# Kernel optimization log

Hardware: AMD Instinct MI355X
Metric: run time of the kernel (lower is better)

Reference implementation:

```python
import jax, jax.numpy as jnp
import numpy as np

NUM_HEADS = 8
NUM_GROUPS = 8
EPS = 1e-5


def group_norm(x, gamma, beta):
    # x: [B, C, H, W], 8 groups over channel dim
    B, C, H, W = x.shape
    xg = x.reshape(B, NUM_GROUPS, C // NUM_GROUPS, H, W)
    mean = xg.mean(axis=(2, 3, 4), keepdims=True)
    var = xg.var(axis=(2, 3, 4), keepdims=True)
    xn = ((xg - mean) * jax.lax.rsqrt(var + EPS)).reshape(B, C, H, W)
    return xn * gamma[None, :, None, None] + beta[None, :, None, None]


def conv1x1(x, w, b):
    # w: [O, C] (1x1 conv kernel squeezed), x: [B, C, H, W]
    return jnp.einsum('oc,bchw->bohw', w, x) + b[None, :, None, None]


def setup_inputs() -> dict:
    key = jax.random.key(0)
    ks = jax.random.split(key, 6)
    B, C, H, W = 16, 512, 32, 32
    x = jax.random.normal(ks[0], (B, C, H, W), dtype=jnp.float32)
    norm_w = jnp.ones((C,), jnp.float32)
    norm_b = jnp.zeros((C,), jnp.float32)
    s = 1.0 / np.sqrt(C)
    qkv_w = jax.random.uniform(ks[1], (3 * C, C), jnp.float32, -s, s)
    qkv_b = jax.random.uniform(ks[2], (3 * C,), jnp.float32, -s, s)
    proj_w = jax.random.uniform(ks[3], (C, C), jnp.float32, -s, s)
    proj_b = jax.random.uniform(ks[4], (C,), jnp.float32, -s, s)
    return {"x": x, "norm_w": norm_w, "norm_b": norm_b,
            "qkv_w": qkv_w, "qkv_b": qkv_b, "proj_w": proj_w, "proj_b": proj_b}


def reference(x, norm_w, norm_b, qkv_w, qkv_b, proj_w, proj_b):
    B, C, H, W = x.shape
    hd = C // NUM_HEADS  # head dim
    h = group_norm(x, norm_w, norm_b)
    qkv = conv1x1(h, qkv_w, qkv_b)                 # [B, 3C, H, W]
    q, k, v = jnp.split(qkv, 3, axis=1)
    q = q.reshape(B, NUM_HEADS, hd, H * W)
    k = k.reshape(B, NUM_HEADS, hd, H * W)
    v = v.reshape(B, NUM_HEADS, hd, H * W)
    scale = hd ** (-0.5)
    attn = jax.nn.softmax(jnp.einsum('bhci,bhcj->bhij', q, k) * scale, axis=-1)
    h = jnp.einsum('bhij,bhcj->bhci', attn, v).reshape(B, C, H, W)
    h = conv1x1(h, proj_w, proj_b)
    return x + h
```

## Files before the change

### kernel.cpp

```cpp
#include <hip/hip_runtime.h>
#include <hip/hip_bf16.h>


typedef __bf16 bf16;
typedef __attribute__((ext_vector_type(8))) __bf16 bf16x8;
typedef __attribute__((ext_vector_type(4))) float f32x4;
typedef __attribute__((ext_vector_type(16))) float f32x16;
typedef __attribute__((ext_vector_type(4))) unsigned int u32x4;

#define SCALE_Q 0.18033688f

__device__ __forceinline__ bf16x8 ld8(const bf16* p) {
    return *reinterpret_cast<const bf16x8*>(p);
}

__device__ __forceinline__ void gl_lds16(const void* g, void* l) {
    __builtin_amdgcn_global_load_lds(
        (const __attribute__((address_space(1))) void*)g,
        (__attribute__((address_space(3))) void*)l, 16, 0, 0);
}

__global__ __launch_bounds__(256) void cvt_gn(const float* __restrict__ qkv_w,
                                              const float* __restrict__ proj_w,
                                              bf16* __restrict__ wdst,
                                              const float* __restrict__ x,
                                              const float* __restrict__ gamma,
                                              const float* __restrict__ beta,
                                              bf16* __restrict__ hnT) {
    __shared__ float tile[64][65];
    __shared__ float ls[4], lq[4];
    __shared__ float2 st;
    int t = threadIdx.x;
    if (blockIdx.x < 1024) {
        const int N1 = 1536 * 512;
        int i = (blockIdx.x * 256 + t) * 4;
        float4 f = (i < N1) ? *reinterpret_cast<const float4*>(qkv_w + i)
                            : *reinterpret_cast<const float4*>(proj_w + (i - N1));
        wdst[i + 0] = (bf16)f.x;
        wdst[i + 1] = (bf16)f.y;
        wdst[i + 2] = (bf16)f.z;
        wdst[i + 3] = (bf16)f.w;
        return;
    }
    int bg = blockIdx.x - 1024;
    int b = bg >> 3, g = bg & 7;
    const float* base = x + (size_t)bg * 65536;
    int wave = t >> 6, lane = t & 63;

    float s = 0.f, sq = 0.f;
    for (int i = t * 4; i < 65536; i += 256 * 4) {
        float4 f = *reinterpret_cast<const float4*>(base + i);
        s += f.x + f.y + f.z + f.w;
        sq += f.x * f.x + f.y * f.y + f.z * f.z + f.w * f.w;
    }
    #pragma unroll
    for (int off = 32; off > 0; off >>= 1) {
        s += __shfl_down(s, off);
        sq += __shfl_down(sq, off);
    }
    if (lane == 0) { ls[wave] = s; lq[wave] = sq; }
    __syncthreads();
    if (t == 0) {
        s = ls[0] + ls[1] + ls[2] + ls[3];
        sq = lq[0] + lq[1] + lq[2] + lq[3];
        float mean = s * (1.f / 65536.f);
        float var = sq * (1.f / 65536.f) - mean * mean;
        st = make_float2(mean, rsqrtf(var + 1e-5f));
    }
    __syncthreads();
    float mean = st.x, rstd = st.y;

    int cl = t & 63;
    float ga = gamma[g * 64 + cl] * rstd;
    float be = beta[g * 64 + cl] - mean * ga;
    for (int pt = 0; pt < 16; pt++) {
        const float* xb = base + pt * 64;
        #pragma unroll
        for (int r = 0; r < 16; r++) {
            int crow = r * 4 + (t >> 6);
            tile[crow][t & 63] = xb[(size_t)crow * 1024 + (t & 63)];
        }
        __syncthreads();
        bf16* ob = hnT + ((size_t)b * 1024 + pt * 64) * 512 + g * 64 + cl;
        #pragma unroll
        for (int r = 0; r < 16; r++) {
            int pl = r * 4 + (t >> 6);
            ob[(size_t)pl * 512] = (bf16)(tile[cl][pl] * ga + be);
        }
        __syncthreads();
    }
}

__device__ __forceinline__ void gemm_stage(const bf16* __restrict__ A,
                                           const bf16* __restrict__ B,
                                           char* smem, int buf,
                                           int m_blk, int n_blk, int k0,
                                           int wave, int lane) {
    char* Al = smem + buf * 32768;
    char* Bl = Al + 16384;
    #pragma unroll
    for (int i = 0; i < 4; i++) {
        int seg = i * 4 + wave;
        int r = seg * 8 + (lane >> 3);
        int cg = (lane & 7) ^ (r & 7);
        gl_lds16((const char*)(A + (size_t)(m_blk + r) * 512 + k0) + cg * 16,
                 Al + seg * 1024);
        gl_lds16((const char*)(B + (size_t)(n_blk + r) * 512 + k0) + cg * 16,
                 Bl + seg * 1024);
    }
}

__device__ __forceinline__ void gemm_compute(const char* smem, int buf,
                                             int wave, int lane,
                                             f32x4 (&acc)[4][4]) {
    const char* Al = smem + buf * 32768;
    const char* Bl = Al + 16384;
    int l15 = lane & 15, hi = lane >> 4;
    int mb = (wave >> 1) * 64, nb = (wave & 1) * 64;
    #pragma unroll
    for (int kc = 0; kc < 2; kc++) {
        int ck = kc * 4 + hi;
        bf16x8 a[4], b[4];
        #pragma unroll
        for (int mf = 0; mf < 4; mf++) {
            int row = mb + mf * 16 + l15;
            a[mf] = *reinterpret_cast<const bf16x8*>(Al + row * 128 + (ck ^ (row & 7)) * 16);
        }
        #pragma unroll
        for (int nf = 0; nf < 4; nf++) {
            int row = nb + nf * 16 + l15;
            b[nf] = *reinterpret_cast<const bf16x8*>(Bl + row * 128 + (ck ^ (row & 7)) * 16);
        }
        #pragma unroll
        for (int mf = 0; mf < 4; mf++)
            #pragma unroll
            for (int nf = 0; nf < 4; nf++)
                acc[mf][nf] = __builtin_amdgcn_mfma_f32_16x16x32_bf16(
                    a[mf], b[nf], acc[mf][nf], 0, 0, 0);
    }
}

#define GEMM_LDS_LOOP(A_, B_, SMEM_)                            \
    f32x4 acc[4][4] = {};                                       \
    {                                                           \
        gemm_stage(A_, B_, SMEM_, 0, m_blk, n_blk, 0, wave, lane); \
        __syncthreads();                                        \
        int buf = 0;                                            \
        for (int ks = 0; ks < 8; ks++) {                        \
            if (ks < 7)                                         \
                gemm_stage(A_, B_, SMEM_, buf ^ 1, m_blk, n_blk, (ks + 1) * 64, wave, lane); \
            gemm_compute(SMEM_, buf, wave, lane, acc);          \
            __syncthreads();                                    \
            buf ^= 1;                                           \
        }                                                       \
    }

__global__ __launch_bounds__(256, 2) void gemm_qkv(const bf16* __restrict__ hnT,
                                                   const bf16* __restrict__ wqkv,
                                                   const float* __restrict__ qkv_b,
                                                   bf16* __restrict__ qk_t,
                                                   bf16* __restrict__ vbuf) {
    __shared__ char smem[65536];
    int b = blockIdx.z;
    int wave = threadIdx.x >> 6, lane = threadIdx.x & 63;
    int l15 = lane & 15;
    int y = blockIdx.y;
    if (y < 8) {
        int m_blk = blockIdx.x * 128;
        int n_blk = y * 128;
        const bf16* A = hnT + (size_t)b * 1024 * 512;
        GEMM_LDS_LOOP(A, wqkv, smem)
        bf16* out = qk_t + (size_t)b * 1024 * 1024;
        int col0 = n_blk + (wave & 1) * 64 + l15;
        int row0 = m_blk + (wave >> 1) * 64 + (lane >> 4) * 4;
        #pragma unroll
        for (int nf = 0; nf < 4; nf++) {
            int col = col0 + nf * 16;
            float bias = qkv_b[col];
            float scl = (col < 512) ? SCALE_Q : 1.0f;
            #pragma unroll
            for (int mf = 0; mf < 4; mf++)
                #pragma unroll
                for (int r = 0; r < 4; r++)
                    out[(size_t)(row0 + mf * 16 + r) * 1024 + col] =
                        (bf16)((acc[mf][nf][r] + bias) * scl);
        }
    } else {
        int m_blk = (y - 8) * 128;
        int n_blk = blockIdx.x * 128;
        const bf16* A = wqkv + (size_t)1024 * 512;
        const bf16* Bm = hnT + (size_t)b * 1024 * 512;
        GEMM_LDS_LOOP(A, Bm, smem)
        bf16* out = vbuf + (size_t)b * 512 * 1024;
        int col0 = n_blk + (wave & 1) * 64 + l15;
        int row0 = m_blk + (wave >> 1) * 64 + (lane >> 4) * 4;
        #pragma unroll
        for (int mf = 0; mf < 4; mf++)
            #pragma unroll
            for (int r = 0; r < 4; r++) {
                int row = row0 + mf * 16 + r;
                float bias = qkv_b[1024 + row];
                #pragma unroll
                for (int nf = 0; nf < 4; nf++)
                    out[(size_t)row * 1024 + col0 + nf * 16] = (bf16)(acc[mf][nf][r] + bias);
            }
    }
}

__global__ __launch_bounds__(256, 2) void gemm_proj(const bf16* __restrict__ wproj,
                                                    const bf16* __restrict__ attnT,
                                                    const float* __restrict__ proj_b,
                                                    const float* __restrict__ x,
                                                    float* __restrict__ out) {
    __shared__ char smem[65536];
    int b = blockIdx.z;
    int wave = threadIdx.x >> 6, lane = threadIdx.x & 63;
    int m_blk = blockIdx.x * 128;
    int n_blk = blockIdx.y * 128;
    const bf16* Bm = attnT + (size_t)b * 1024 * 512;
    GEMM_LDS_LOOP(wproj, Bm, smem)
    const float* xb = x + (size_t)b * 512 * 1024;
    float* ob = out + (size_t)b * 512 * 1024;
    int l15 = lane & 15;
    int col0 = n_blk + (wave & 1) * 64 + l15;
    int row0 = m_blk + (wave >> 1) * 64 + (lane >> 4) * 4;
    #pragma unroll
    for (int mf = 0; mf < 4; mf++)
        #pragma unroll
        for (int r = 0; r < 4; r++) {
            int row = row0 + mf * 16 + r;
            float bias = proj_b[row];
            #pragma unroll
            for (int nf = 0; nf < 4; nf++) {
                size_t idx = (size_t)row * 1024 + col0 + nf * 16;
                ob[idx] = acc[mf][nf][r] + bias + xb[idx];
            }
        }
}

__global__ __launch_bounds__(256, 2) void attn_kernel(const bf16* __restrict__ qk_t,
                                                      const bf16* __restrict__ vbuf,
                                                      bf16* __restrict__ attnT) {
    int flat = blockIdx.x;
    int it = flat >> 7;
    int bh = flat & 127;
    int b = bh >> 3, h = bh & 7;
    int wave = threadIdx.x >> 6, lane = threadIdx.x & 63;
    int l31 = lane & 31, hi = lane >> 5;
    int i0 = it * 128 + wave * 32;
    const bf16* qkb = qk_t + (size_t)b * 1024 * 1024;
    const bf16* kbase = qkb + 512 + h * 64;
    const bf16* vb = vbuf + ((size_t)b * 512 + h * 64) * 1024;

    __shared__ __align__(16) char smem[32768];

    bf16x8 bq[4];
    #pragma unroll
    for (int kc = 0; kc < 4; kc++)
        bq[kc] = ld8(qkb + (size_t)(i0 + l31) * 1024 + h * 64 + kc * 16 + hi * 8);

    f32x16 oacc[2] = {};
    f32x4 l4 = {};

    int srow = wave * 8 + (lane >> 3);
    int cg = (lane & 7) ^ (lane >> 3);
    const char* kp = (const char*)kbase + (size_t)srow * 2048 + cg * 16;
    const char* vp = (const char*)vb + (size_t)srow * 2048 + cg * 16;
    char* ldsK = smem + wave * 1024;

#define ATTN_STAGE(BUFI)                                     \
    {                                                        \
        gl_lds16(kp,         ldsK + (BUFI) * 16384);         \
        gl_lds16(kp + 65536, ldsK + (BUFI) * 16384 + 4096);  \
        gl_lds16(vp,         ldsK + (BUFI) * 16384 + 8192);  \
        gl_lds16(vp + 65536, ldsK + (BUFI) * 16384 + 12288); \
        kp += 131072;                                        \
        vp += 128;                                           \
    }

    int rx = l31 & 7;
    int vaddr[4];
    #pragma unroll
    for (int k = 0; k < 4; k++) vaddr[k] = l31 * 128 + (((k * 2 + hi) ^ rx) * 16);

#define ATTN_COMPUTE(BUFC)                                                              \
    {                                                                                   \
        bf16x8 kf[2][4];                                                                \
        _Pragma("unroll")                                                               \
        for (int jb = 0; jb < 2; jb++)                                                  \
            _Pragma("unroll")                                                           \
            for (int kc = 0; kc < 4; kc++)                                              \
                kf[jb][kc] = *reinterpret_cast<const bf16x8*>(                          \
                    smem + (BUFC) * 16384 + jb * 4096 + vaddr[kc]);                     \
        f32x16 s[2] = {};                                                               \
        _Pragma("unroll")                                                               \
        for (int kc = 0; kc < 4; kc++) {                                                \
            s[0] = __builtin_amdgcn_mfma_f32_32x32x16_bf16(kf[0][kc], bq[kc], s[0], 0, 0, 0); \
            s[1] = __builtin_amdgcn_mfma_f32_32x32x16_bf16(kf[1][kc], bq[kc], s[1], 0, 0, 0); \
        }                                                                               \
        bf16x8 vf[2][4];                                                                \
        _Pragma("unroll")                                                               \
        for (int df = 0; df < 2; df++)                                                  \
            _Pragma("unroll")                                                           \
            for (int ks = 0; ks < 4; ks++)                                              \
                vf[df][ks] = *reinterpret_cast<const bf16x8*>(                          \
                    smem + (BUFC) * 16384 + 8192 + df * 4096 + vaddr[ks]);              \
        unsigned int pk0[2][4], pk1[2][4];                                              \
        _Pragma("unroll")                                                               \
        for (int jb = 0; jb < 2; jb++)                                                  \
            _Pragma("unroll")                                                           \
            for (int m = 0; m < 4; m++) {                                               \
                float e0 = exp2f(s[jb][m * 4 + 0]);                                     \
                float e1 = exp2f(s[jb][m * 4 + 1]);                                     \
                float e2 = exp2f(s[jb][m * 4 + 2]);                                     \
                float e3 = exp2f(s[jb][m * 4 + 3]);                                     \
                f32x4 ev = {e0, e1, e2, e3};                                            \
                l4 += ev;                                                               \
                asm("v_cvt_pk_bf16_f32 %0, %1, %2" : "=v"(pk0[jb][m]) : "v"(e0), "v"(e1)); \
                asm("v_cvt_pk_bf16_f32 %0, %1, %2" : "=v"(pk1[jb][m]) : "v"(e2), "v"(e3)); \
            }                                                                           \
        bf16x8 af[4];                                                                   \
        _Pragma("unroll")                                                               \
        for (int jb = 0; jb < 2; jb++)                                                  \
            _Pragma("unroll")                                                           \
            for (int tt = 0; tt < 2; tt++) {                                            \
                unsigned int a0 = pk0[jb][tt * 2], b0 = pk0[jb][tt * 2 + 1];            \
                unsigned int a1 = pk1[jb][tt * 2], b1 = pk1[jb][tt * 2 + 1];            \
                asm("v_permlane32_swap_b32 %0, %1" : "+v"(a0), "+v"(b0));               \
                asm("v_permlane32_swap_b32 %0, %1" : "+v"(a1), "+v"(b1));               \
                u32x4 w = {a0, a1, b0, b1};                                             \
                af[jb * 2 + tt] = __builtin_bit_cast(bf16x8, w);                        \
            }                                                                           \
        _Pragma("unroll")                                                               \
        for (int ks = 0; ks < 4; ks++) {                                                \
            oacc[0] = __builtin_amdgcn_mfma_f32_32x32x16_bf16(af[ks], vf[0][ks], oacc[0], 0, 0, 0); \
            oacc[1] = __builtin_amdgcn_mfma_f32_32x32x16_bf16(af[ks], vf[1][ks], oacc[1], 0, 0, 0); \
        }                                                                               \
    }

    ATTN_STAGE(0)

    for (int t = 0; t < 16; t += 2) {
        asm volatile("" ::: "memory");
        __builtin_amdgcn_s_barrier();
        ATTN_STAGE(1)
        asm volatile("s_waitcnt vmcnt(4)" ::: "memory");
        __builtin_amdgcn_s_barrier();
        asm volatile("" ::: "memory");
        ATTN_COMPUTE(0)

        asm volatile("" ::: "memory");
        __builtin_amdgcn_s_barrier();
        if (t < 14) {
            ATTN_STAGE(0)
            asm volatile("s_waitcnt vmcnt(4)" ::: "memory");
        } else {
            asm volatile("s_waitcnt vmcnt(0)" ::: "memory");
        }
        __builtin_amdgcn_s_barrier();
        asm volatile("" ::: "memory");
        ATTN_COMPUTE(1)
    }
#undef ATTN_STAGE
#undef ATTN_COMPUTE

    float l_part = (l4[0] + l4[1]) + (l4[2] + l4[3]);
    float lsum = l_part + __shfl_xor(l_part, 32);
    float inv = 1.f / lsum;

    __syncthreads();

    bf16* O_l = (bf16*)smem;
    #pragma unroll
    for (int reg = 0; reg < 16; reg++) {
        int qrow = (reg & 3) + 8 * (reg >> 2) + 4 * hi;
        float iv = __shfl(inv, qrow);
        O_l[(wave * 32 + qrow) * 72 + l31]      = (bf16)(oacc[0][reg] * iv);
        O_l[(wave * 32 + qrow) * 72 + 32 + l31] = (bf16)(oacc[1][reg] * iv);
    }
    __syncthreads();
    {
        int tt = threadIdx.x;
        int il = tt >> 1, half = tt & 1;
        const bf16* lsrc = O_l + il * 72 + half * 32;
        bf16* gdst = attnT + ((size_t)b * 1024 + it * 128 + il) * 512 + h * 64 + half * 32;
        #pragma unroll
        for (int k = 0; k < 4; k++)
            *reinterpret_cast<bf16x8*>(gdst + k * 8) =
                *reinterpret_cast<const bf16x8*>(lsrc + k * 8);
    }
}

extern "C" void kernel_launch(void* const* d_in, const int* in_sizes, int n_in,
                              void* d_out, int out_size, void* d_ws, size_t ws_size,
                              hipStream_t stream) {
    (void)in_sizes; (void)n_in; (void)out_size; (void)ws_size;
    const float* x      = (const float*)d_in[0];
    const float* norm_w = (const float*)d_in[1];
    const float* norm_b = (const float*)d_in[2];
    const float* qkv_w  = (const float*)d_in[3];
    const float* qkv_b  = (const float*)d_in[4];
    const float* proj_w = (const float*)d_in[5];
    const float* proj_b = (const float*)d_in[6];
    float* out = (float*)d_out;

    char* w = (char*)d_ws;
    bf16* wqkv  = (bf16*)w;
    bf16* wproj = wqkv + (size_t)1536 * 512;
    bf16* hnT   = wproj + (size_t)512 * 512;
    bf16* qk_t  = hnT + (size_t)16 * 1024 * 512;
    bf16* vbuf  = qk_t + (size_t)16 * 1024 * 1024;
    bf16* attnT = vbuf + (size_t)16 * 512 * 1024;

    cvt_gn<<<1152, 256, 0, stream>>>(qkv_w, proj_w, wqkv, x, norm_w, norm_b, hnT);
    gemm_qkv<<<dim3(8, 12, 16), 256, 0, stream>>>(hnT, wqkv, qkv_b, qk_t, vbuf);
    attn_kernel<<<1024, 256, 0, stream>>>(qk_t, vbuf, attnT);
    gemm_proj<<<dim3(4, 8, 16), 256, 0, stream>>>(wproj, attnT, proj_b, x, out);
}
```

Baseline: 141.6 us.

## Process two 32-row query tiles per wave to reuse K/V tiles in attention

```diff
diff --git a/kernel.cpp b/kernel.cpp
--- a/kernel.cpp
+++ b/kernel.cpp
@@ -247,20 +247,23 @@
     int b = bh >> 3, h = bh & 7;
     int wave = threadIdx.x >> 6, lane = threadIdx.x & 63;
     int l31 = lane & 31, hi = lane >> 5;
-    int i0 = it * 128 + wave * 32;
+    int i0 = it * 256 + wave * 64;
     const bf16* qkb = qk_t + (size_t)b * 1024 * 1024;
     const bf16* kbase = qkb + 512 + h * 64;
     const bf16* vb = vbuf + ((size_t)b * 512 + h * 64) * 1024;
 
-    __shared__ __align__(16) char smem[32768];
-
-    bf16x8 bq[4];
-    #pragma unroll
-    for (int kc = 0; kc < 4; kc++)
-        bq[kc] = ld8(qkb + (size_t)(i0 + l31) * 1024 + h * 64 + kc * 16 + hi * 8);
-
-    f32x16 oacc[2] = {};
-    f32x4 l4 = {};
+    __shared__ __align__(16) char smem[36864];
+
+    bf16x8 bq[2][4];
+    #pragma unroll
+    for (int qt = 0; qt < 2; qt++)
+        #pragma unroll
+        for (int kc = 0; kc < 4; kc++)
+            bq[qt][kc] = ld8(qkb + (size_t)(i0 + qt * 32 + l31) * 1024 +
+                             h * 64 + kc * 16 + hi * 8);
+
+    f32x16 oacc[2][2] = {};
+    f32x4 l4[2] = {};
 
     int srow = wave * 8 + (lane >> 3);
     int cg = (lane & 7) ^ (lane >> 3);
@@ -292,11 +295,40 @@
             for (int kc = 0; kc < 4; kc++)                                              \
                 kf[jb][kc] = *reinterpret_cast<const bf16x8*>(                          \
                     smem + (BUFC) * 16384 + jb * 4096 + vaddr[kc]);                     \
-        f32x16 s[2] = {};                                                               \
+        bf16x8 af[2][4];                                                                \
         _Pragma("unroll")                                                               \
-        for (int kc = 0; kc < 4; kc++) {                                                \
-            s[0] = __builtin_amdgcn_mfma_f32_32x32x16_bf16(kf[0][kc], bq[kc], s[0], 0, 0, 0); \
-            s[1] = __builtin_amdgcn_mfma_f32_32x32x16_bf16(kf[1][kc], bq[kc], s[1], 0, 0, 0); \
+        for (int qt = 0; qt < 2; qt++) {                                                \
+            f32x16 s[2] = {};                                                           \
+            _Pragma("unroll")                                                           \
+            for (int kc = 0; kc < 4; kc++) {                                            \
+                s[0] = __builtin_amdgcn_mfma_f32_32x32x16_bf16(kf[0][kc], bq[qt][kc], s[0], 0, 0, 0); \
+                s[1] = __builtin_amdgcn_mfma_f32_32x32x16_bf16(kf[1][kc], bq[qt][kc], s[1], 0, 0, 0); \
+            }                                                                           \
+            unsigned int pk0[2][4], pk1[2][4];                                          \
+            _Pragma("unroll")                                                           \
+            for (int jb = 0; jb < 2; jb++)                                              \
+                _Pragma("unroll")                                                       \
+                for (int m = 0; m < 4; m++) {                                           \
+                    float e0 = exp2f(s[jb][m * 4 + 0]);                                 \
+                    float e1 = exp2f(s[jb][m * 4 + 1]);                                 \
+                    float e2 = exp2f(s[jb][m * 4 + 2]);                                 \
+                    float e3 = exp2f(s[jb][m * 4 + 3]);                                 \
+                    f32x4 ev = {e0, e1, e2, e3};                                        \
+                    l4[qt] += ev;                                                       \
+                    asm("v_cvt_pk_bf16_f32 %0, %1, %2" : "=v"(pk0[jb][m]) : "v"(e0), "v"(e1)); \
+                    asm("v_cvt_pk_bf16_f32 %0, %1, %2" : "=v"(pk1[jb][m]) : "v"(e2), "v"(e3)); \
+                }                                                                       \
+            _Pragma("unroll")                                                           \
+            for (int jb = 0; jb < 2; jb++)                                              \
+                _Pragma("unroll")                                                       \
+                for (int tt = 0; tt < 2; tt++) {                                        \
+                    unsigned int a0 = pk0[jb][tt * 2], b0 = pk0[jb][tt * 2 + 1];        \
+                    unsigned int a1 = pk1[jb][tt * 2], b1 = pk1[jb][tt * 2 + 1];        \
+                    asm("v_permlane32_swap_b32 %0, %1" : "+v"(a0), "+v"(b0));           \
+                    asm("v_permlane32_swap_b32 %0, %1" : "+v"(a1), "+v"(b1));           \
+                    u32x4 w = {a0, a1, b0, b1};                                         \
+                    af[qt][jb * 2 + tt] = __builtin_bit_cast(bf16x8, w);                \
+                }                                                                       \
         }                                                                               \
         bf16x8 vf[2][4];                                                                \
         _Pragma("unroll")                                                               \
@@ -305,36 +337,12 @@
             for (int ks = 0; ks < 4; ks++)                                              \
                 vf[df][ks] = *reinterpret_cast<const bf16x8*>(                          \
                     smem + (BUFC) * 16384 + 8192 + df * 4096 + vaddr[ks]);              \
-        unsigned int pk0[2][4], pk1[2][4];                                              \
-        _Pragma("unroll")                                                               \
-        for (int jb = 0; jb < 2; jb++)                                                  \
-            _Pragma("unroll")                                                           \
-            for (int m = 0; m < 4; m++) {                                               \
-                float e0 = exp2f(s[jb][m * 4 + 0]);                                     \
-                float e1 = exp2f(s[jb][m * 4 + 1]);                                     \
-                float e2 = exp2f(s[jb][m * 4 + 2]);                                     \
-                float e3 = exp2f(s[jb][m * 4 + 3]);                                     \
-                f32x4 ev = {e0, e1, e2, e3};                                            \
-                l4 += ev;                                                               \
-                asm("v_cvt_pk_bf16_f32 %0, %1, %2" : "=v"(pk0[jb][m]) : "v"(e0), "v"(e1)); \
-                asm("v_cvt_pk_bf16_f32 %0, %1, %2" : "=v"(pk1[jb][m]) : "v"(e2), "v"(e3)); \
-            }                                                                           \
-        bf16x8 af[4];                                                                   \
-        _Pragma("unroll")                                                               \
-        for (int jb = 0; jb < 2; jb++)                                                  \
-            _Pragma("unroll")                                                           \
-            for (int tt = 0; tt < 2; tt++) {                                            \
-                unsigned int a0 = pk0[jb][tt * 2], b0 = pk0[jb][tt * 2 + 1];            \
-                unsigned int a1 = pk1[jb][tt * 2], b1 = pk1[jb][tt * 2 + 1];            \
-                asm("v_permlane32_swap_b32 %0, %1" : "+v"(a0), "+v"(b0));               \
-                asm("v_permlane32_swap_b32 %0, %1" : "+v"(a1), "+v"(b1));               \
-                u32x4 w = {a0, a1, b0, b1};                                             \
-                af[jb * 2 + tt] = __builtin_bit_cast(bf16x8, w);                        \
-            }                                                                           \
         _Pragma("unroll")                                                               \
         for (int ks = 0; ks < 4; ks++) {                                                \
-            oacc[0] = __builtin_amdgcn_mfma_f32_32x32x16_bf16(af[ks], vf[0][ks], oacc[0], 0, 0, 0); \
-            oacc[1] = __builtin_amdgcn_mfma_f32_32x32x16_bf16(af[ks], vf[1][ks], oacc[1], 0, 0, 0); \
+            oacc[0][0] = __builtin_amdgcn_mfma_f32_32x32x16_bf16(af[0][ks], vf[0][ks], oacc[0][0], 0, 0, 0); \
+            oacc[0][1] = __builtin_amdgcn_mfma_f32_32x32x16_bf16(af[0][ks], vf[1][ks], oacc[0][1], 0, 0, 0); \
+            oacc[1][0] = __builtin_amdgcn_mfma_f32_32x32x16_bf16(af[1][ks], vf[0][ks], oacc[1][0], 0, 0, 0); \
+            oacc[1][1] = __builtin_amdgcn_mfma_f32_32x32x16_bf16(af[1][ks], vf[1][ks], oacc[1][1], 0, 0, 0); \
         }                                                                               \
     }
 
@@ -364,30 +372,42 @@
 #undef ATTN_STAGE
 #undef ATTN_COMPUTE
 
-    float l_part = (l4[0] + l4[1]) + (l4[2] + l4[3]);
-    float lsum = l_part + __shfl_xor(l_part, 32);
-    float inv = 1.f / lsum;
+    float inv[2];
+    #pragma unroll
+    for (int qt = 0; qt < 2; qt++) {
+        float lp = (l4[qt][0] + l4[qt][1]) + (l4[qt][2] + l4[qt][3]);
+        float lsum = lp + __shfl_xor(lp, 32);
+        inv[qt] = 1.f / lsum;
+    }
 
     __syncthreads();
 
     bf16* O_l = (bf16*)smem;
     #pragma unroll
-    for (int reg = 0; reg < 16; reg++) {
-        int qrow = (reg & 3) + 8 * (reg >> 2) + 4 * hi;
-        float iv = __shfl(inv, qrow);
-        O_l[(wave * 32 + qrow) * 72 + l31]      = (bf16)(oacc[0][reg] * iv);
-        O_l[(wave * 32 + qrow) * 72 + 32 + l31] = (bf16)(oacc[1][reg] * iv);
-    }
+    for (int qt = 0; qt < 2; qt++)
+        #pragma unroll
+        for (int reg = 0; reg < 16; reg++) {
+            int qrow = (reg & 3) + 8 * (reg >> 2) + 4 * hi;
+            float iv = __shfl(inv[qt], qrow);
+            int row = wave * 64 + qt * 32 + qrow;
+            O_l[row * 72 + l31]      = (bf16)(oacc[qt][0][reg] * iv);
+            O_l[row * 72 + 32 + l31] = (bf16)(oacc[qt][1][reg] * iv);
+        }
     __syncthreads();
     {
         int tt = threadIdx.x;
-        int il = tt >> 1, half = tt & 1;
-        const bf16* lsrc = O_l + il * 72 + half * 32;
-        bf16* gdst = attnT + ((size_t)b * 1024 + it * 128 + il) * 512 + h * 64 + half * 32;
-        #pragma unroll
-        for (int k = 0; k < 4; k++)
-            *reinterpret_cast<bf16x8*>(gdst + k * 8) =
-                *reinterpret_cast<const bf16x8*>(lsrc + k * 8);
+        #pragma unroll
+        for (int k2 = 0; k2 < 2; k2++) {
+            int p = tt + 256 * k2;
+            int il = p >> 1, half = p & 1;
+            const bf16* lsrc = O_l + il * 72 + half * 32;
+            bf16* gdst = attnT + ((size_t)b * 1024 + it * 256 + il) * 512 +
+                         h * 64 + half * 32;
+            #pragma unroll
+            for (int k = 0; k < 4; k++)
+                *reinterpret_cast<bf16x8*>(gdst + k * 8) =
+                    *reinterpret_cast<const bf16x8*>(lsrc + k * 8);
+        }
     }
 }
 
@@ -414,6 +434,6 @@
 
     cvt_gn<<<1152, 256, 0, stream>>>(qkv_w, proj_w, wqkv, x, norm_w, norm_b, hnT);
     gemm_qkv<<<dim3(8, 12, 16), 256, 0, stream>>>(hnT, wqkv, qkv_b, qk_t, vbuf);
-    attn_kernel<<<1024, 256, 0, stream>>>(qk_t, vbuf, attnT);
+    attn_kernel<<<512, 256, 0, stream>>>(qk_t, vbuf, attnT);
     gemm_proj<<<dim3(4, 8, 16), 256, 0, stream>>>(wproj, attnT, proj_b, x, out);
 }
```

Result: no change. 142.8 us (+0.9%).
